# Optimization experiments

Hardware: AMD Instinct MI355X
Metric: run time of the kernel (lower is better)

## Reference

```python
import jax, jax.numpy as jnp
import numpy as np

IGNORE_INDEX = -100


def setup_inputs() -> dict:
    key = jax.random.key(0)
    k1, k2 = jax.random.split(key)
    logits = jax.random.normal(k1, (8, 19, 512, 512), dtype=jnp.float32)
    labels = jax.random.randint(k2, (8, 512, 512), 0, 19, dtype=jnp.int64)
    return {"logits": logits, "labels": labels}


def reference(logits, labels):
    # Lovasz-Softmax loss (CoinCheung/pytorch-loss LovaszSoftmaxV3, reduction='mean').
    n, c, h, w = logits.shape
    lg = jnp.moveaxis(logits, 1, 0).reshape(c, -1).astype(jnp.float32)  # [C, P]
    lb = labels.reshape(-1)  # [P]
    valid = (lb != IGNORE_INDEX)

    probs = jax.nn.softmax(lg, axis=0)  # [C, P]
    # one-hot labels, zeroed at ignored pixels
    onehot = ((jnp.arange(c)[:, None] == lb[None, :]) & valid[None, :]).astype(jnp.float32)

    errs = jnp.abs(onehot - probs)
    # push ignored pixels to the end of the descending sort with sentinel -1
    errs = jnp.where(valid[None, :], errs, jnp.float32(-1.0))

    order = jnp.argsort(-errs, axis=1)  # descending sort per class
    errs_sort = jnp.take_along_axis(errs, order, axis=1)
    oh_sort = jnp.take_along_axis(onehot, order, axis=1)

    # Lovasz extension gradient (jacc), computed without autodiff flow
    n_pos = oh_sort.sum(axis=1, keepdims=True)
    inter = n_pos - jnp.cumsum(oh_sort, axis=1)
    union = n_pos + jnp.cumsum(1.0 - oh_sort, axis=1)
    jacc = 1.0 - inter / union
    jacc = jnp.concatenate([jacc[:, :1], jacc[:, 1:] - jacc[:, :-1]], axis=1)

    # ignored pixels have errs_sort = -1 -> relu zeroes their contribution
    losses = jnp.sum(jax.nn.relu(errs_sort) * jacc, axis=1)  # per-class [C]
    return losses.mean()
```

## Files before the change

### kernel.cpp

```cpp
#include <hip/hip_runtime.h>
#include <hip/hip_bf16.h>

#define NCLASS 19
#define BINS 512
#define NB (NCLASS * BINS)
#define NREP 4
#define RPAD 8
#define RSTRIDE (NB + RPAD)
#define SLICES 8
#define IGNORE_IDX (-100)
#define HW_SHIFT 18
#define HW_C (1 << HW_SHIFT)

__global__ void __launch_bounds__(1024, 1) hist_lds4r(
    const float* __restrict__ logits, const int* __restrict__ labels,
    unsigned* __restrict__ copies, int P, int ppb) {
  extern __shared__ unsigned sh[];
  for (int i = threadIdx.x; i < NREP * RSTRIDE; i += 1024) sh[i] = 0u;
  __syncthreads();

  const int rep = (threadIdx.x & 3) * RSTRIDE;

  int p0 = blockIdx.x * ppb;
  int p1 = min(P, p0 + ppb);
  for (int p = p0 + (int)threadIdx.x * 2; p < p1; p += 1024 * 2) {
    int n = p >> HW_SHIFT;
    int hw = p & (HW_C - 1);
    const float* lp = logits + (((size_t)n * NCLASS) << HW_SHIFT) + hw;

    float v[NCLASS][2];
    float m0 = -3.4e38f, m1 = -3.4e38f;
#pragma unroll
    for (int c = 0; c < NCLASS; ++c) {
      float2 q = *(const float2*)(lp + ((size_t)c << HW_SHIFT));
      v[c][0] = q.x; v[c][1] = q.y;
      m0 = fmaxf(m0, q.x); m1 = fmaxf(m1, q.y);
    }
    float s0 = 0.f, s1 = 0.f;
#pragma unroll
    for (int c = 0; c < NCLASS; ++c) {
      v[c][0] = __expf(v[c][0] - m0); s0 += v[c][0];
      v[c][1] = __expf(v[c][1] - m1); s1 += v[c][1];
    }
    float inv0 = 1.0f / s0, inv1 = 1.0f / s1;

    int2 lb2 = *(const int2*)(labels + p);
    int lb0 = lb2.x, lb1 = lb2.y;

#pragma unroll
    for (int c = 0; c < NCLASS; ++c) {
      if (lb0 != IGNORE_IDX) {
        float prob = v[c][0] * inv0;
        bool pos = (c == lb0);
        float e = pos ? (1.0f - prob) : prob;
        int b = min(BINS - 1, (int)(e * (float)BINS));
        atomicAdd(&sh[rep + (c << 9) + b], pos ? 0x10000u : 1u);
      }
      if (lb1 != IGNORE_IDX) {
        float prob = v[c][1] * inv1;
        bool pos = (c == lb1);
        float e = pos ? (1.0f - prob) : prob;
        int b = min(BINS - 1, (int)(e * (float)BINS));
        atomicAdd(&sh[rep + (c << 9) + b], pos ? 0x10000u : 1u);
      }
    }
  }
  __syncthreads();

  unsigned* dst = copies + (size_t)blockIdx.x * NB;
  for (int i = threadIdx.x; i < NB; i += 1024)
    dst[i] = sh[i] + sh[RSTRIDE + i] + sh[2 * RSTRIDE + i] +
             sh[3 * RSTRIDE + i];
}

__global__ void __launch_bounds__(256) reduce_part(
    const unsigned* __restrict__ copies, unsigned long long* __restrict__ part,
    int R) {
  const int nblk = NB / 256;
  int s = blockIdx.x / nblk;
  int blk = blockIdx.x - s * nblk;
  int cb = blk * 256 + threadIdx.x;
  unsigned long long acc = 0;
  for (int r = s; r < R; r += SLICES) {
    unsigned v = copies[(size_t)r * NB + cb];
    acc += ((unsigned long long)(v >> 16) << 32) |
           (unsigned long long)(v & 0xffffu);
  }
  part[(size_t)s * NB + cb] = acc;
}

__global__ void __launch_bounds__(256) scan19_fold(
    const unsigned long long* __restrict__ part, float* __restrict__ partial) {
  int c = blockIdx.x;
  __shared__ unsigned long long bins[BINS];
  __shared__ unsigned long long arr[256];
  __shared__ unsigned long long wsum[4];
  __shared__ float fsum[4];
  int tid = threadIdx.x;

  for (int i = tid; i < BINS; i += 256) {
    unsigned long long a = 0;
#pragma unroll
    for (int s = 0; s < SLICES; ++s) a += part[(size_t)s * NB + c * BINS + i];
    bins[i] = a;
  }
  __syncthreads();

  unsigned long long t = 0;
  for (int i = tid; i < BINS; i += 256) t += bins[i];
  for (int off = 32; off > 0; off >>= 1) t += __shfl_down(t, off, 64);
  int lane = tid & 63, w = tid >> 6;
  if (lane == 0) wsum[w] = t;
  __syncthreads();
  unsigned long long total = wsum[0] + wsum[1] + wsum[2] + wsum[3];
  float nPos = (float)(unsigned)(total >> 32);

  unsigned long long above = 0;
  float acc = 0.f;
  for (int r = BINS / 256 - 1; r >= 0; --r) {
    arr[tid] = bins[r * 256 + tid];
    __syncthreads();
    for (int off = 1; off < 256; off <<= 1) {
      unsigned long long add = (tid + off < 256) ? arr[tid + off] : 0ull;
      __syncthreads();
      arr[tid] += add;
      __syncthreads();
    }
    unsigned long long suff = arr[tid] + above;
    unsigned long long rowTot = arr[0];
    __syncthreads();

    int gb = r * 256 + tid;
    if (gb >= 1) {
      float CP = (float)(unsigned)(suff >> 32);
      float CN = (float)(unsigned)(suff & 0xffffffffull);
      float uni = nPos + CN;
      if (uni > 0.f) acc += 1.0f - (nPos - CP) / uni;
    }
    above += rowTot;
  }

  for (int off = 32; off > 0; off >>= 1) acc += __shfl_down(acc, off, 64);
  if (lane == 0) fsum[w] = acc;
  __syncthreads();
  if (tid == 0) partial[c] = fsum[0] + fsum[1] + fsum[2] + fsum[3];
}

__global__ void __launch_bounds__(64) lovasz_final(
    const float* __restrict__ partial, float* __restrict__ out, int n,
    float scale) {
  float acc = 0.f;
  for (int i = threadIdx.x; i < n; i += 64) acc += partial[i];
  for (int off = 32; off > 0; off >>= 1) acc += __shfl_down(acc, off, 64);
  if (threadIdx.x == 0) out[0] = acc * scale;
}

extern "C" void kernel_launch(void* const* d_in, const int* in_sizes, int n_in,
                              void* d_out, int out_size, void* d_ws,
                              size_t ws_size, hipStream_t stream) {
  const float* logits = (const float*)d_in[0];
  const int* labels = (const int*)d_in[1];
  float* out = (float*)d_out;

  const int P = in_sizes[1];

  int R = 256;
  while (R > 32 &&
         (size_t)R * NB * 4 + (size_t)SLICES * NB * 8 + 4096 > ws_size)
    R >>= 1;
  int ppb = ((P + R - 1) / R + 2047) & ~2047;

  char* ws = (char*)d_ws;
  unsigned* copies = (unsigned*)ws;
  unsigned long long* part = (unsigned long long*)(ws + (size_t)R * NB * 4);
  float* partial = (float*)(part + (size_t)SLICES * NB);

  size_t ldsBytes = (size_t)NREP * RSTRIDE * 4;

  hist_lds4r<<<R, 1024, ldsBytes, stream>>>(logits, labels, copies, P, ppb);
  reduce_part<<<SLICES * (NB / 256), 256, 0, stream>>>(copies, part, R);
  scan19_fold<<<NCLASS, 256, 0, stream>>>(part, partial);
  lovasz_final<<<1, 64, 0, stream>>>(partial, out, NCLASS,
                                     1.0f / ((float)BINS * (float)NCLASS));
}
```

Baseline: 52.00 us.

## Halve LDS histogram replicas and process one pixel per thread for occupancy

```diff
diff --git a/kernel.cpp b/kernel.cpp
--- a/kernel.cpp
+++ b/kernel.cpp
@@ -4,7 +4,7 @@
 #define NCLASS 19
 #define BINS 512
 #define NB (NCLASS * BINS)
-#define NREP 4
+#define NREP 2
 #define RPAD 8
 #define RSTRIDE (NB + RPAD)
 #define SLICES 8
@@ -12,65 +12,53 @@
 #define HW_SHIFT 18
 #define HW_C (1 << HW_SHIFT)
 
-__global__ void __launch_bounds__(1024, 1) hist_lds4r(
+__global__ void __launch_bounds__(1024, 8) hist_occ(
     const float* __restrict__ logits, const int* __restrict__ labels,
     unsigned* __restrict__ copies, int P, int ppb) {
   extern __shared__ unsigned sh[];
   for (int i = threadIdx.x; i < NREP * RSTRIDE; i += 1024) sh[i] = 0u;
   __syncthreads();
 
-  const int rep = (threadIdx.x & 3) * RSTRIDE;
+  const int rep = (threadIdx.x & 1) * RSTRIDE;
 
   int p0 = blockIdx.x * ppb;
   int p1 = min(P, p0 + ppb);
-  for (int p = p0 + (int)threadIdx.x * 2; p < p1; p += 1024 * 2) {
+  for (int p = p0 + (int)threadIdx.x; p < p1; p += 1024) {
     int n = p >> HW_SHIFT;
     int hw = p & (HW_C - 1);
     const float* lp = logits + (((size_t)n * NCLASS) << HW_SHIFT) + hw;
 
-    float v[NCLASS][2];
-    float m0 = -3.4e38f, m1 = -3.4e38f;
+    float v[NCLASS];
+    float m = -3.4e38f;
 #pragma unroll
     for (int c = 0; c < NCLASS; ++c) {
-      float2 q = *(const float2*)(lp + ((size_t)c << HW_SHIFT));
-      v[c][0] = q.x; v[c][1] = q.y;
-      m0 = fmaxf(m0, q.x); m1 = fmaxf(m1, q.y);
+      v[c] = lp[(size_t)c << HW_SHIFT];
+      m = fmaxf(m, v[c]);
     }
-    float s0 = 0.f, s1 = 0.f;
+    float s = 0.f;
 #pragma unroll
     for (int c = 0; c < NCLASS; ++c) {
-      v[c][0] = __expf(v[c][0] - m0); s0 += v[c][0];
-      v[c][1] = __expf(v[c][1] - m1); s1 += v[c][1];
+      v[c] = __expf(v[c] - m);
+      s += v[c];
     }
-    float inv0 = 1.0f / s0, inv1 = 1.0f / s1;
+    float inv = 1.0f / s;
 
-    int2 lb2 = *(const int2*)(labels + p);
-    int lb0 = lb2.x, lb1 = lb2.y;
+    int lb = labels[p];
+    if (lb == IGNORE_IDX) continue;
 
 #pragma unroll
     for (int c = 0; c < NCLASS; ++c) {
-      if (lb0 != IGNORE_IDX) {
-        float prob = v[c][0] * inv0;
-        bool pos = (c == lb0);
-        float e = pos ? (1.0f - prob) : prob;
-        int b = min(BINS - 1, (int)(e * (float)BINS));
-        atomicAdd(&sh[rep + (c << 9) + b], pos ? 0x10000u : 1u);
-      }
-      if (lb1 != IGNORE_IDX) {
-        float prob = v[c][1] * inv1;
-        bool pos = (c == lb1);
-        float e = pos ? (1.0f - prob) : prob;
-        int b = min(BINS - 1, (int)(e * (float)BINS));
-        atomicAdd(&sh[rep + (c << 9) + b], pos ? 0x10000u : 1u);
-      }
+      float prob = v[c] * inv;
+      bool pos = (c == lb);
+      float e = pos ? (1.0f - prob) : prob;
+      int b = min(BINS - 1, (int)(e * (float)BINS));
+      atomicAdd(&sh[rep + (c << 9) + b], pos ? 0x10000u : 1u);
     }
   }
   __syncthreads();
 
   unsigned* dst = copies + (size_t)blockIdx.x * NB;
-  for (int i = threadIdx.x; i < NB; i += 1024)
-    dst[i] = sh[i] + sh[RSTRIDE + i] + sh[2 * RSTRIDE + i] +
-             sh[3 * RSTRIDE + i];
+  for (int i = threadIdx.x; i < NB; i += 1024) dst[i] = sh[i] + sh[RSTRIDE + i];
 }
 
 __global__ void __launch_bounds__(256) reduce_part(
@@ -164,11 +152,11 @@
 
   const int P = in_sizes[1];
 
-  int R = 256;
+  int R = 512;
   while (R > 32 &&
          (size_t)R * NB * 4 + (size_t)SLICES * NB * 8 + 4096 > ws_size)
     R >>= 1;
-  int ppb = ((P + R - 1) / R + 2047) & ~2047;
+  int ppb = (P + R - 1) / R;
 
   char* ws = (char*)d_ws;
   unsigned* copies = (unsigned*)ws;
@@ -177,7 +165,7 @@
 
   size_t ldsBytes = (size_t)NREP * RSTRIDE * 4;
 
-  hist_lds4r<<<R, 1024, ldsBytes, stream>>>(logits, labels, copies, P, ppb);
+  hist_occ<<<R, 1024, ldsBytes, stream>>>(logits, labels, copies, P, ppb);
   reduce_part<<<SLICES * (NB / 256), 256, 0, stream>>>(copies, part, R);
   scan19_fold<<<NCLASS, 256, 0, stream>>>(part, partial);
   lovasz_final<<<1, 64, 0, stream>>>(partial, out, NCLASS,
```

Measured after the change: 58.55 us. +12.6%, slower.
